# Performance work log

Hardware: AMD Instinct MI355X
Metric: run time of the kernel (lower is better)

Reference implementation:

```python
import jax, jax.numpy as jnp
import numpy as np

RTOL = 1e-3
ATOL = 1e-4
DT0 = 0.05      # initial step size
N_ITER = 64     # fixed budget of adaptive-solver iterations (accepted or rejected)
SAFETY, MIN_FAC, MAX_FAC = 0.9, 0.2, 5.0

# Dormand-Prince 5(4) Butcher tableau
_A = (
    (),
    (1/5,),
    (3/40, 9/40),
    (44/45, -56/15, 32/9),
    (19372/6561, -25360/2187, 64448/6561, -212/729),
    (9017/3168, -355/33, 46732/5247, 49/176, -5103/18656),
    (35/384, 0.0, 500/1113, 125/192, -2187/6784, 11/84),
)
_C = (0.0, 1/5, 3/10, 4/5, 8/9, 1.0, 1.0)
_B5 = (35/384, 0.0, 500/1113, 125/192, -2187/6784, 11/84, 0.0)
_B4 = (5179/57600, 0.0, 7571/16695, 393/640, -92097/339200, 187/2100, 1/40)


def setup_inputs() -> dict:
    key = jax.random.key(0)
    k0, k1, k2 = jax.random.split(key, 3)
    B, F, H = 256, 256, 1024
    x0 = jax.random.normal(k0, (B, F), jnp.float32)
    W1 = jax.random.normal(k1, (F + 1, H), jnp.float32) * (1.0 / np.sqrt(F + 1))
    b1 = jnp.zeros((H,), jnp.float32)
    W2 = jax.random.normal(k2, (H, F), jnp.float32) * (1.0 / np.sqrt(H))
    b2 = jnp.zeros((F,), jnp.float32)
    return {"x0": x0, "W1": W1, "b1": b1, "W2": W2, "b2": b2}


def _vf(x, t, W1, b1, W2, b2):
    # f(x, t): MLP on [x; t] -- last row of W1 multiplies the time input
    h = jnp.tanh(x @ W1[:-1] + t * W1[-1] + b1)
    return h @ W2 + b2


def _odeint_dopri5(x0, W1, b1, W2, b2):
    def body(carry, _):
        t, x, dt = carry
        done = t >= 1.0
        dt_c = jnp.maximum(jnp.minimum(dt, 1.0 - t), 0.0)  # clip to domain end
        # 7 RK stages
        ks = []
        for i in range(7):
            xi = x
            for j in range(i):
                if _A[i][j] != 0.0:
                    xi = xi + (dt_c * _A[i][j]) * ks[j]
            ks.append(_vf(xi, t + _C[i] * dt_c, W1, b1, W2, b2))
        # 5th-order solution and embedded 4th-order error estimate
        x5 = x
        err = jnp.zeros_like(x)
        for j in range(7):
            if _B5[j] != 0.0:
                x5 = x5 + (dt_c * _B5[j]) * ks[j]
            d = _B5[j] - _B4[j]
            if d != 0.0:
                err = err + (dt_c * d) * ks[j]
        scale = ATOL + RTOL * jnp.maximum(jnp.abs(x), jnp.abs(x5))
        err_norm = jnp.sqrt(jnp.mean((err / scale) ** 2))
        accept = err_norm <= 1.0
        factor = jnp.clip(SAFETY * (err_norm + 1e-10) ** (-0.2), MIN_FAC, MAX_FAC)
        t_n = jnp.where(done, t, jnp.where(accept, t + dt_c, t))
        x_n = jnp.where(jnp.logical_or(done, jnp.logical_not(accept)), x, x5)
        dt_n = jnp.where(done, dt, dt_c * factor)
        return (t_n, x_n, dt_n), None

    carry0 = (jnp.float32(0.0), x0, jnp.float32(DT0))
    (_, xf, _), _ = jax.lax.scan(body, carry0, None, length=N_ITER)
    # trajectory at t_span = [0, 1] -> (2, batch, features)
    return jnp.stack([x0, xf], axis=0)


def reference(x0, W1, b1, W2, b2):
    return _odeint_dopri5(x0, W1, b1, W2, b2)
```

## Files before the change

kernel.cpp:

```cpp
#include <hip/hip_runtime.h>
#include <hip/hip_cooperative_groups.h>
#include <cstdint>

namespace cg = cooperative_groups;


typedef _Float16 f16x8 __attribute__((ext_vector_type(8)));
typedef float f32x4 __attribute__((ext_vector_type(4)));

#define SMEM_BYTES 152640

#define STAMP_OFF (2u * 1024u * 1024u)
#define SLOT_OFF  (STAMP_OFF + 4096u)

union U64H4 { unsigned long long u; _Float16 h[4]; };

__device__ __forceinline__ float fast_tanh(float v) {
  float e = __builtin_amdgcn_exp2f(v * 2.88539008177793f);
  return fmaf(-2.0f, __builtin_amdgcn_rcpf(e + 1.0f), 1.0f);
}

extern "C" __global__ void __launch_bounds__(256, 1) neural_ode_dopri5(
    const float* __restrict__ x0g, const float* __restrict__ W1,
    const float* __restrict__ b1, const float* __restrict__ W2,
    const float* __restrict__ b2, float* __restrict__ out,
    unsigned long long* __restrict__ partB, unsigned* __restrict__ stamps,
    float* __restrict__ errSlots) {
  cg::grid_group gridg = cg::this_grid();
  const int tid = threadIdx.x;
  const int bx = blockIdx.x;
  const int g = bx & 31;
  const int m = bx >> 5;
  const int w = tid >> 6, lane = tid & 63, n16 = lane & 15, q = lane >> 4;
  const int r = tid >> 5, fb = tid & 31;

  extern __shared__ char smem[];
  _Float16* W1s  = (_Float16*)smem;
  _Float16* W2s  = (_Float16*)(smem + 67584);
  _Float16* xi_s = (_Float16*)(smem + 137216);
  _Float16* h_s  = (_Float16*)(smem + 145664);
  float* sw1t   = (float*)(smem + 150016);
  float* sb1c   = sw1t + 128;
  float* sbias1 = sb1c + 128;
  float* sb2    = sbias1 + 128;
  float* sred   = sb2 + 256;
  float* sbc    = sred + 4;

  if (bx == 0) {
    for (int i = tid; i < 512; i += 256) stamps[i] = 0u;
    for (int i = tid; i < 2048; i += 256) errSlots[i] = -1.0f;
  }
  for (int kk = 0; kk < 128; ++kk) {
    const int k = 2 * kk + (tid >> 7), c = tid & 127;
    W1s[c * 264 + k] = (_Float16)W1[k * 1024 + m * 128 + c];
  }
  for (int kk = 0; kk < 128; ++kk)
    W2s[tid * 136 + kk] = (_Float16)W2[(m * 128 + kk) * 256 + tid];
  if (tid < 128) {
    sw1t[tid] = W1[256 * 1024 + m * 128 + tid];
    sb1c[tid] = b1[m * 128 + tid];
  }
  sb2[tid] = b2[tid];
  for (int i = tid; i < 16 * 264; i += 256) xi_s[i] = (_Float16)0.0f;
  for (int i = tid; i < 16 * 136; i += 256) h_s[i] = (_Float16)0.0f;
  gridg.sync();

  const float* xrow = x0g + (8 * g + r) * 256 + fb * 8;
  float x[8];
  {
    float4 v0 = ((const float4*)xrow)[0], v1 = ((const float4*)xrow)[1];
    x[0] = v0.x; x[1] = v0.y; x[2] = v0.z; x[3] = v0.w;
    x[4] = v1.x; x[5] = v1.y; x[6] = v1.z; x[7] = v1.w;
  }
  float ks[7][8];
  unsigned phase = 0;

  auto stage_eval = [&](const float* xi, float ti, float* kout) {
    ++phase;
    const unsigned buf = phase & 1u;
    if (tid < 128) sbias1[tid] = fmaf(ti, sw1t[tid], sb1c[tid]);
    f16x8 xv;
#pragma unroll
    for (int j = 0; j < 8; ++j) xv[j] = (_Float16)xi[j];
    *(f16x8*)(xi_s + r * 264 + fb * 8) = xv;
    __syncthreads();

    f32x4 acc1[2];
#pragma unroll
    for (int tt = 0; tt < 2; ++tt) {
      const float bb = sbias1[(2 * w + tt) * 16 + n16];
      acc1[tt] = (f32x4){bb, bb, bb, bb};
    }
#pragma unroll
    for (int kk = 0; kk < 8; ++kk) {
      const f16x8 av = *(const f16x8*)(xi_s + n16 * 264 + kk * 32 + q * 8);
#pragma unroll
      for (int tt = 0; tt < 2; ++tt) {
        const f16x8 bv =
            *(const f16x8*)(W1s + ((2 * w + tt) * 16 + n16) * 264 + kk * 32 + q * 8);
        acc1[tt] = __builtin_amdgcn_mfma_f32_16x16x32_f16(av, bv, acc1[tt], 0, 0, 0);
      }
    }
#pragma unroll
    for (int tt = 0; tt < 2; ++tt) {
      const int c = (2 * w + tt) * 16 + n16;
#pragma unroll
      for (int reg = 0; reg < 4; ++reg)
        h_s[(q * 4 + reg) * 136 + c] = (_Float16)fast_tanh(acc1[tt][reg]);
    }
    __syncthreads();

    f32x4 acc2[4];
#pragma unroll
    for (int tt = 0; tt < 4; ++tt) acc2[tt] = (f32x4){0.f, 0.f, 0.f, 0.f};
#pragma unroll
    for (int kk = 0; kk < 4; ++kk) {
      const f16x8 av = *(const f16x8*)(h_s + n16 * 136 + kk * 32 + q * 8);
#pragma unroll
      for (int tt = 0; tt < 4; ++tt) {
        const f16x8 bv =
            *(const f16x8*)(W2s + ((w * 4 + tt) * 16 + n16) * 136 + kk * 32 + q * 8);
        acc2[tt] = __builtin_amdgcn_mfma_f32_16x16x32_f16(av, bv, acc2[tt], 0, 0, 0);
      }
    }
    _Float16* stag = xi_s;
    if (q < 2) {
#pragma unroll
      for (int tt = 0; tt < 4; ++tt) {
        const int c = (w * 4 + tt) * 16 + n16;
#pragma unroll
        for (int reg = 0; reg < 4; ++reg)
          stag[(q * 4 + reg) * 264 + c] = (_Float16)acc2[tt][reg];
      }
    }
    __syncthreads();
    {
      const unsigned long long* srcp =
          (const unsigned long long*)(stag + r * 264 + fb * 8);
      unsigned long long u0 = srcp[0], u1 = srcp[1];
      unsigned long long* dst =
          partB + (buf << 17) + (bx << 9) + (r << 6) + (fb << 1);
      __hip_atomic_store(dst, u0, __ATOMIC_RELAXED, __HIP_MEMORY_SCOPE_AGENT);
      __hip_atomic_store(dst + 1, u1, __ATOMIC_RELAXED, __HIP_MEMORY_SCOPE_AGENT);
    }
    __syncthreads();
    if (tid == 0)
      __hip_atomic_store(&stamps[g * 16 + m], phase, __ATOMIC_RELAXED,
                         __HIP_MEMORY_SCOPE_AGENT);
    if (w == 0) {
      for (;;) {
        unsigned v = phase;
        if (lane < 8)
          v = __hip_atomic_load(&stamps[g * 16 + lane], __ATOMIC_RELAXED,
                                __HIP_MEMORY_SCOPE_AGENT);
        if (__all(v >= phase)) break;
      }
    }
    __syncthreads();
    float kacc[8];
    {
      const float4* sb2v = (const float4*)(sb2 + fb * 8);
      float4 bA = sb2v[0], bB = sb2v[1];
      kacc[0] = bA.x; kacc[1] = bA.y; kacc[2] = bA.z; kacc[3] = bA.w;
      kacc[4] = bB.x; kacc[5] = bB.y; kacc[6] = bB.z; kacc[7] = bB.w;
    }
    const int gbase = (buf << 17) + (r << 6) + (fb << 1);
#pragma unroll
    for (int mm = 0; mm < 8; ++mm) {
      const unsigned long long* pp = partB + gbase + ((mm * 32 + g) << 9);
      U64H4 ua, ub;
      ua.u = __hip_atomic_load(pp, __ATOMIC_RELAXED, __HIP_MEMORY_SCOPE_AGENT);
      ub.u = __hip_atomic_load(pp + 1, __ATOMIC_RELAXED, __HIP_MEMORY_SCOPE_AGENT);
#pragma unroll
      for (int j = 0; j < 4; ++j) {
        kacc[j] += (float)ua.h[j];
        kacc[4 + j] += (float)ub.h[j];
      }
    }
#pragma unroll
    for (int j = 0; j < 8; ++j) kout[j] = kacc[j];
  };

  const float AB[6][6] = {
      {(float)(1.0 / 5.0), 0, 0, 0, 0, 0},
      {(float)(3.0 / 40.0), (float)(9.0 / 40.0), 0, 0, 0, 0},
      {(float)(44.0 / 45.0), (float)(-56.0 / 15.0), (float)(32.0 / 9.0), 0, 0, 0},
      {(float)(19372.0 / 6561.0), (float)(-25360.0 / 2187.0),
       (float)(64448.0 / 6561.0), (float)(-212.0 / 729.0), 0, 0},
      {(float)(9017.0 / 3168.0), (float)(-355.0 / 33.0),
       (float)(46732.0 / 5247.0), (float)(49.0 / 176.0),
       (float)(-5103.0 / 18656.0), 0},
      {(float)(35.0 / 384.0), 0.0f, (float)(500.0 / 1113.0),
       (float)(125.0 / 192.0), (float)(-2187.0 / 6784.0), (float)(11.0 / 84.0)}};
  const float CC[7] = {0.0f, (float)(1.0 / 5.0), (float)(3.0 / 10.0),
                       (float)(4.0 / 5.0), (float)(8.0 / 9.0), 1.0f, 1.0f};
  const float DD[7] = {(float)(35.0 / 384.0 - 5179.0 / 57600.0), 0.0f,
                       (float)(500.0 / 1113.0 - 7571.0 / 16695.0),
                       (float)(125.0 / 192.0 - 393.0 / 640.0),
                       (float)(-2187.0 / 6784.0 + 92097.0 / 339200.0),
                       (float)(11.0 / 84.0 - 187.0 / 2100.0),
                       (float)(-1.0 / 40.0)};

  float t = 0.0f, dt = 0.05f;
  stage_eval(x, 0.0f, ks[0]);

  for (int it = 0; it < 64; ++it) {
    if (t >= 1.0f) break;
    const float dt_c = fmaxf(fminf(dt, 1.0f - t), 0.0f);

    float x5[8];
#pragma unroll
    for (int s = 1; s <= 6; ++s) {
      float xi[8];
#pragma unroll
      for (int j = 0; j < 8; ++j) {
        float v = x[j];
#pragma unroll
        for (int p = 0; p < 6; ++p)
          if (p < s) v = fmaf(dt_c * AB[s - 1][p], ks[p][j], v);
        xi[j] = v;
        if (s == 6) x5[j] = v;
      }
      stage_eval(xi, fmaf(CC[s], dt_c, t), ks[s]);
    }

    if (m == 0) {
      float loc = 0.0f;
#pragma unroll
      for (int j = 0; j < 8; ++j) {
        float e = 0.0f;
#pragma unroll
        for (int s = 0; s < 7; ++s) e = fmaf(dt_c * DD[s], ks[s][j], e);
        const float scale = fmaf(1e-3f, fmaxf(fabsf(x[j]), fabsf(x5[j])), 1e-4f);
        const float rr = e / scale;
        loc = fmaf(rr, rr, loc);
      }
#pragma unroll
      for (int o = 32; o > 0; o >>= 1) loc += __shfl_down(loc, o);
      if (lane == 0) sred[w] = loc;
      __syncthreads();
      if (tid == 0) {
        const float s4 = sred[0] + sred[1] + sred[2] + sred[3];
        __hip_atomic_store(&errSlots[it * 32 + g], s4, __ATOMIC_RELAXED,
                           __HIP_MEMORY_SCOPE_AGENT);
      }
    }
    if (w == 0) {
      for (;;) {
        float v = 0.0f;
        bool okl = true;
        if (lane < 32) {
          v = __hip_atomic_load(&errSlots[it * 32 + lane], __ATOMIC_RELAXED,
                                __HIP_MEMORY_SCOPE_AGENT);
          okl = (v >= 0.0f);
        }
        if (__all(okl)) {
#pragma unroll
          for (int o = 32; o > 0; o >>= 1) v += __shfl_down(v, o);
          if (lane == 0) sbc[0] = v;
          break;
        }
      }
    }
    __syncthreads();
    const float total = sbc[0];
    const float err_norm = sqrtf(total * (1.0f / 65536.0f));
    const bool accept = err_norm <= 1.0f;
    float factor = 0.9f * powf(err_norm + 1e-10f, -0.2f);
    factor = fminf(fmaxf(factor, 0.2f), 5.0f);
    if (accept) {
      t = t + dt_c;
#pragma unroll
      for (int j = 0; j < 8; ++j) { x[j] = x5[j]; ks[0][j] = ks[6][j]; }
    }
    dt = dt_c * factor;
  }

  if (m == 0) {
    float4* o0 = (float4*)(out + (8 * g + r) * 256 + fb * 8);
    const float4* xr = (const float4*)xrow;
    o0[0] = xr[0]; o0[1] = xr[1];
    float4 a0, a1;
    a0.x = x[0]; a0.y = x[1]; a0.z = x[2]; a0.w = x[3];
    a1.x = x[4]; a1.y = x[5]; a1.z = x[6]; a1.w = x[7];
    float4* o1 = (float4*)(out + 65536 + (8 * g + r) * 256 + fb * 8);
    o1[0] = a0; o1[1] = a1;
  }
}

extern "C" void kernel_launch(void* const* d_in, const int* in_sizes, int n_in,
                              void* d_out, int out_size, void* d_ws,
                              size_t ws_size, hipStream_t stream) {
  const float* x0 = (const float*)d_in[0];
  const float* W1 = (const float*)d_in[1];
  const float* b1 = (const float*)d_in[2];
  const float* W2 = (const float*)d_in[3];
  const float* b2 = (const float*)d_in[4];
  float* out = (float*)d_out;
  char* ws = (char*)d_ws;
  unsigned long long* partB = (unsigned long long*)ws;
  unsigned* stamps = (unsigned*)(ws + STAMP_OFF);
  float* errSlots = (float*)(ws + SLOT_OFF);

  hipFuncSetAttribute((const void*)neural_ode_dopri5,
                      hipFuncAttributeMaxDynamicSharedMemorySize, SMEM_BYTES);

  void* args[] = {&x0, &W1, &b1, &W2, &b2, &out, &partB, &stamps, &errSlots};
  hipLaunchCooperativeKernel((void*)neural_ode_dopri5, dim3(256), dim3(256),
                             args, SMEM_BYTES, stream);
}
```

Before: 208.6 us.

## Embed phase tags in partial-sum words to replace stamp barrier with per-slot polling

```diff
diff --git a/kernel.cpp b/kernel.cpp
--- a/kernel.cpp
+++ b/kernel.cpp
@@ -10,22 +10,24 @@
 
 #define SMEM_BYTES 152640
 
-#define STAMP_OFF (2u * 1024u * 1024u)
-#define SLOT_OFF  (STAMP_OFF + 4096u)
-
-union U64H4 { unsigned long long u; _Float16 h[4]; };
+#define PART_OFF 8192u
+
+union H1U { unsigned short u; _Float16 h; };
 
 __device__ __forceinline__ float fast_tanh(float v) {
   float e = __builtin_amdgcn_exp2f(v * 2.88539008177793f);
   return fmaf(-2.0f, __builtin_amdgcn_rcpf(e + 1.0f), 1.0f);
 }
 
+__device__ __forceinline__ float f16b(unsigned b) {
+  H1U x; x.u = (unsigned short)b; return (float)x.h;
+}
+
 extern "C" __global__ void __launch_bounds__(256, 1) neural_ode_dopri5(
     const float* __restrict__ x0g, const float* __restrict__ W1,
     const float* __restrict__ b1, const float* __restrict__ W2,
     const float* __restrict__ b2, float* __restrict__ out,
-    unsigned long long* __restrict__ partB, unsigned* __restrict__ stamps,
-    float* __restrict__ errSlots) {
+    unsigned long long* __restrict__ partB, float* __restrict__ errSlots) {
   cg::grid_group gridg = cg::this_grid();
   const int tid = threadIdx.x;
   const int bx = blockIdx.x;
@@ -46,10 +48,8 @@
   float* sred   = sb2 + 256;
   float* sbc    = sred + 4;
 
-  if (bx == 0) {
-    for (int i = tid; i < 512; i += 256) stamps[i] = 0u;
+  if (bx == 0)
     for (int i = tid; i < 2048; i += 256) errSlots[i] = -1.0f;
-  }
   for (int kk = 0; kk < 128; ++kk) {
     const int k = 2 * kk + (tid >> 7), c = tid & 127;
     W1s[c * 264 + k] = (_Float16)W1[k * 1024 + m * 128 + c];
@@ -134,29 +134,29 @@
       }
     }
     __syncthreads();
+
     {
       const unsigned long long* srcp =
           (const unsigned long long*)(stag + r * 264 + fb * 8);
-      unsigned long long u0 = srcp[0], u1 = srcp[1];
+      const unsigned long long s0 = srcp[0], s1 = srcp[1];
+      const unsigned long long st2 =
+          ((unsigned long long)phase << 48) | ((unsigned long long)phase << 16);
+      const unsigned long long w0 =
+          (s0 & 0xFFFFull) | (((s0 >> 16) & 0xFFFFull) << 32) | st2;
+      const unsigned long long w1 =
+          ((s0 >> 32) & 0xFFFFull) | (((s0 >> 48) & 0xFFFFull) << 32) | st2;
+      const unsigned long long w2 =
+          (s1 & 0xFFFFull) | (((s1 >> 16) & 0xFFFFull) << 32) | st2;
+      const unsigned long long w3 =
+          ((s1 >> 32) & 0xFFFFull) | (((s1 >> 48) & 0xFFFFull) << 32) | st2;
       unsigned long long* dst =
-          partB + (buf << 17) + (bx << 9) + (r << 6) + (fb << 1);
-      __hip_atomic_store(dst, u0, __ATOMIC_RELAXED, __HIP_MEMORY_SCOPE_AGENT);
-      __hip_atomic_store(dst + 1, u1, __ATOMIC_RELAXED, __HIP_MEMORY_SCOPE_AGENT);
-    }
-    __syncthreads();
-    if (tid == 0)
-      __hip_atomic_store(&stamps[g * 16 + m], phase, __ATOMIC_RELAXED,
-                         __HIP_MEMORY_SCOPE_AGENT);
-    if (w == 0) {
-      for (;;) {
-        unsigned v = phase;
-        if (lane < 8)
-          v = __hip_atomic_load(&stamps[g * 16 + lane], __ATOMIC_RELAXED,
-                                __HIP_MEMORY_SCOPE_AGENT);
-        if (__all(v >= phase)) break;
-      }
-    }
-    __syncthreads();
+          partB + ((((buf << 8) + bx) << 10) + (r << 7) + (fb << 2));
+      __hip_atomic_store(dst + 0, w0, __ATOMIC_RELAXED, __HIP_MEMORY_SCOPE_AGENT);
+      __hip_atomic_store(dst + 1, w1, __ATOMIC_RELAXED, __HIP_MEMORY_SCOPE_AGENT);
+      __hip_atomic_store(dst + 2, w2, __ATOMIC_RELAXED, __HIP_MEMORY_SCOPE_AGENT);
+      __hip_atomic_store(dst + 3, w3, __ATOMIC_RELAXED, __HIP_MEMORY_SCOPE_AGENT);
+    }
+
     float kacc[8];
     {
       const float4* sb2v = (const float4*)(sb2 + fb * 8);
@@ -164,19 +164,44 @@
       kacc[0] = bA.x; kacc[1] = bA.y; kacc[2] = bA.z; kacc[3] = bA.w;
       kacc[4] = bB.x; kacc[5] = bB.y; kacc[6] = bB.z; kacc[7] = bB.w;
     }
-    const int gbase = (buf << 17) + (r << 6) + (fb << 1);
-#pragma unroll
-    for (int mm = 0; mm < 8; ++mm) {
-      const unsigned long long* pp = partB + gbase + ((mm * 32 + g) << 9);
-      U64H4 ua, ub;
-      ua.u = __hip_atomic_load(pp, __ATOMIC_RELAXED, __HIP_MEMORY_SCOPE_AGENT);
-      ub.u = __hip_atomic_load(pp + 1, __ATOMIC_RELAXED, __HIP_MEMORY_SCOPE_AGENT);
-#pragma unroll
-      for (int j = 0; j < 4; ++j) {
-        kacc[j] += (float)ua.h[j];
-        kacc[4 + j] += (float)ub.h[j];
-      }
-    }
+    const unsigned ph = phase;
+    unsigned pend = 0xFFu;
+    do {
+#pragma unroll
+      for (int mm = 0; mm < 8; ++mm) {
+        if (!(pend & (1u << mm))) continue;
+        const unsigned long long* pp =
+            partB +
+            ((((buf << 8) + (mm << 5) + g) << 10) + (r << 7) + (fb << 2));
+        const unsigned long long a0 =
+            __hip_atomic_load(pp + 0, __ATOMIC_RELAXED, __HIP_MEMORY_SCOPE_AGENT);
+        const unsigned long long a1 =
+            __hip_atomic_load(pp + 1, __ATOMIC_RELAXED, __HIP_MEMORY_SCOPE_AGENT);
+        const unsigned long long a2 =
+            __hip_atomic_load(pp + 2, __ATOMIC_RELAXED, __HIP_MEMORY_SCOPE_AGENT);
+        const unsigned long long a3 =
+            __hip_atomic_load(pp + 3, __ATOMIC_RELAXED, __HIP_MEMORY_SCOPE_AGENT);
+        const bool ok = (((unsigned)(a0 >> 16) & 0xFFFFu) == ph) &
+                        ((unsigned)(a0 >> 48) == ph) &
+                        (((unsigned)(a1 >> 16) & 0xFFFFu) == ph) &
+                        ((unsigned)(a1 >> 48) == ph) &
+                        (((unsigned)(a2 >> 16) & 0xFFFFu) == ph) &
+                        ((unsigned)(a2 >> 48) == ph) &
+                        (((unsigned)(a3 >> 16) & 0xFFFFu) == ph) &
+                        ((unsigned)(a3 >> 48) == ph);
+        if (ok) {
+          kacc[0] += f16b((unsigned)a0 & 0xFFFFu);
+          kacc[1] += f16b((unsigned)(a0 >> 32) & 0xFFFFu);
+          kacc[2] += f16b((unsigned)a1 & 0xFFFFu);
+          kacc[3] += f16b((unsigned)(a1 >> 32) & 0xFFFFu);
+          kacc[4] += f16b((unsigned)a2 & 0xFFFFu);
+          kacc[5] += f16b((unsigned)(a2 >> 32) & 0xFFFFu);
+          kacc[6] += f16b((unsigned)a3 & 0xFFFFu);
+          kacc[7] += f16b((unsigned)(a3 >> 32) & 0xFFFFu);
+          pend &= ~(1u << mm);
+        }
+      }
+    } while (pend);
 #pragma unroll
     for (int j = 0; j < 8; ++j) kout[j] = kacc[j];
   };
@@ -298,14 +323,13 @@
   const float* b2 = (const float*)d_in[4];
   float* out = (float*)d_out;
   char* ws = (char*)d_ws;
-  unsigned long long* partB = (unsigned long long*)ws;
-  unsigned* stamps = (unsigned*)(ws + STAMP_OFF);
-  float* errSlots = (float*)(ws + SLOT_OFF);
+  float* errSlots = (float*)ws;
+  unsigned long long* partB = (unsigned long long*)(ws + PART_OFF);
 
   hipFuncSetAttribute((const void*)neural_ode_dopri5,
                       hipFuncAttributeMaxDynamicSharedMemorySize, SMEM_BYTES);
 
-  void* args[] = {&x0, &W1, &b1, &W2, &b2, &out, &partB, &stamps, &errSlots};
+  void* args[] = {&x0, &W1, &b1, &W2, &b2, &out, &partB, &errSlots};
   hipLaunchCooperativeKernel((void*)neural_ode_dopri5, dim3(256), dim3(256),
                              args, SMEM_BYTES, stream);
 }
```

New measurement: 293.2 us. +40.6%, slower.

## Use per-wave staging and an LDS counter to drop block barriers before stamp publish

Applied to the files above, without the earlier changes.

```diff
diff --git a/kernel.cpp b/kernel.cpp
--- a/kernel.cpp
+++ b/kernel.cpp
@@ -8,7 +8,7 @@
 typedef _Float16 f16x8 __attribute__((ext_vector_type(8)));
 typedef float f32x4 __attribute__((ext_vector_type(4)));
 
-#define SMEM_BYTES 152640
+#define SMEM_BYTES 157248
 
 #define STAMP_OFF (2u * 1024u * 1024u)
 #define SLOT_OFF  (STAMP_OFF + 4096u)
@@ -39,17 +39,20 @@
   _Float16* W2s  = (_Float16*)(smem + 67584);
   _Float16* xi_s = (_Float16*)(smem + 137216);
   _Float16* h_s  = (_Float16*)(smem + 145664);
-  float* sw1t   = (float*)(smem + 150016);
+  _Float16* stag = (_Float16*)(smem + 150016);
+  float* sw1t   = (float*)(smem + 154624);
   float* sb1c   = sw1t + 128;
   float* sbias1 = sb1c + 128;
   float* sb2    = sbias1 + 128;
   float* sred   = sb2 + 256;
   float* sbc    = sred + 4;
+  unsigned* scount = (unsigned*)(sbc + 1);
 
   if (bx == 0) {
     for (int i = tid; i < 512; i += 256) stamps[i] = 0u;
     for (int i = tid; i < 2048; i += 256) errSlots[i] = -1.0f;
   }
+  if (tid == 0) *scount = 0u;
   for (int kk = 0; kk < 128; ++kk) {
     const int k = 2 * kk + (tid >> 7), c = tid & 127;
     W1s[c * 264 + k] = (_Float16)W1[k * 1024 + m * 128 + c];
@@ -123,30 +126,33 @@
         acc2[tt] = __builtin_amdgcn_mfma_f32_16x16x32_f16(av, bv, acc2[tt], 0, 0, 0);
       }
     }
-    _Float16* stag = xi_s;
+    _Float16* stagW = stag + w * (8 * 72);
     if (q < 2) {
 #pragma unroll
       for (int tt = 0; tt < 4; ++tt) {
-        const int c = (w * 4 + tt) * 16 + n16;
+        const int c = tt * 16 + n16;
 #pragma unroll
         for (int reg = 0; reg < 4; ++reg)
-          stag[(q * 4 + reg) * 264 + c] = (_Float16)acc2[tt][reg];
-      }
-    }
-    __syncthreads();
+          stagW[(q * 4 + reg) * 72 + c] = (_Float16)acc2[tt][reg];
+      }
+    }
     {
+      const int row = lane >> 3, c8 = lane & 7;
       const unsigned long long* srcp =
-          (const unsigned long long*)(stag + r * 264 + fb * 8);
+          (const unsigned long long*)(stagW + row * 72 + c8 * 8);
       unsigned long long u0 = srcp[0], u1 = srcp[1];
       unsigned long long* dst =
-          partB + (buf << 17) + (bx << 9) + (r << 6) + (fb << 1);
+          partB + (buf << 17) + (bx << 9) + (row << 6) + (w << 4) + (c8 << 1);
       __hip_atomic_store(dst, u0, __ATOMIC_RELAXED, __HIP_MEMORY_SCOPE_AGENT);
       __hip_atomic_store(dst + 1, u1, __ATOMIC_RELAXED, __HIP_MEMORY_SCOPE_AGENT);
     }
-    __syncthreads();
-    if (tid == 0)
-      __hip_atomic_store(&stamps[g * 16 + m], phase, __ATOMIC_RELAXED,
-                         __HIP_MEMORY_SCOPE_AGENT);
+    asm volatile("s_waitcnt vmcnt(0)" ::: "memory");
+    if (lane == 0) {
+      const unsigned old = atomicAdd(scount, 1u);
+      if (old == 4u * phase - 1u)
+        __hip_atomic_store(&stamps[g * 16 + m], phase, __ATOMIC_RELAXED,
+                           __HIP_MEMORY_SCOPE_AGENT);
+    }
     if (w == 0) {
       for (;;) {
         unsigned v = phase;
@@ -157,6 +163,15 @@
       }
     }
     __syncthreads();
+
+    unsigned long long va[8][2];
+    const int gbase = (buf << 17) + (r << 6) + (fb << 1);
+#pragma unroll
+    for (int mm = 0; mm < 8; ++mm) {
+      const unsigned long long* pp = partB + gbase + ((mm * 32 + g) << 9);
+      va[mm][0] = __hip_atomic_load(pp, __ATOMIC_RELAXED, __HIP_MEMORY_SCOPE_AGENT);
+      va[mm][1] = __hip_atomic_load(pp + 1, __ATOMIC_RELAXED, __HIP_MEMORY_SCOPE_AGENT);
+    }
     float kacc[8];
     {
       const float4* sb2v = (const float4*)(sb2 + fb * 8);
@@ -164,13 +179,10 @@
       kacc[0] = bA.x; kacc[1] = bA.y; kacc[2] = bA.z; kacc[3] = bA.w;
       kacc[4] = bB.x; kacc[5] = bB.y; kacc[6] = bB.z; kacc[7] = bB.w;
     }
-    const int gbase = (buf << 17) + (r << 6) + (fb << 1);
 #pragma unroll
     for (int mm = 0; mm < 8; ++mm) {
-      const unsigned long long* pp = partB + gbase + ((mm * 32 + g) << 9);
       U64H4 ua, ub;
-      ua.u = __hip_atomic_load(pp, __ATOMIC_RELAXED, __HIP_MEMORY_SCOPE_AGENT);
-      ub.u = __hip_atomic_load(pp + 1, __ATOMIC_RELAXED, __HIP_MEMORY_SCOPE_AGENT);
+      ua.u = va[mm][0]; ub.u = va[mm][1];
 #pragma unroll
       for (int j = 0; j < 4; ++j) {
         kacc[j] += (float)ua.h[j];
```

Measured after the change: 228.6 us. +9.6%, slower.
